# Optimization experiments

Hardware: AMD Instinct MI355X
Metric: run time of the kernel (lower is better)

Reference implementation:

```python
import jax, jax.numpy as jnp
import numpy as np

H = 50  # hidden_layer_size

def _lstm_layer(x, Wih, Whh, bih, bhh):
    # x: [B, T, D_in]; Wih: [4H, D_in]; Whh: [4H, H]; biases: [4H]
    # Precompute input contribution to all gates for every timestep.
    xg = jnp.einsum('btd,gd->btg', x, Wih) + bih + bhh  # [B, T, 4H]
    xg = jnp.transpose(xg, (1, 0, 2))                   # [T, B, 4H] for scan
    B = x.shape[0]
    h0 = jnp.zeros((B, H), x.dtype)
    c0 = jnp.zeros((B, H), x.dtype)

    def step(carry, xt):
        h, c = carry
        g = xt + h @ Whh.T                              # [B, 4H]
        i, f, gg, o = jnp.split(g, 4, axis=-1)          # PyTorch gate order i,f,g,o
        i = jax.nn.sigmoid(i)
        f = jax.nn.sigmoid(f)
        gg = jnp.tanh(gg)
        o = jax.nn.sigmoid(o)
        c = f * c + i * gg
        h = o * jnp.tanh(c)
        return (h, c), h

    (_, _), hs = jax.lax.scan(step, (h0, c0), xg)       # hs: [T, B, H]
    return jnp.transpose(hs, (1, 0, 2))                 # [B, T, H]


def setup_inputs() -> dict:
    key = jax.random.key(0)
    ks = jax.random.split(key, 11)
    B, T, D = 4096, 512, 1
    s = 1.0 / np.sqrt(H)  # PyTorch LSTM init scale
    inp = {
        'x': jax.random.normal(ks[0], (B, T, D), jnp.float32),
        'W_ih0': jax.random.uniform(ks[1], (4 * H, D), jnp.float32, -s, s),
        'W_hh0': jax.random.uniform(ks[2], (4 * H, H), jnp.float32, -s, s),
        'b_ih0': jax.random.uniform(ks[3], (4 * H,), jnp.float32, -s, s),
        'b_hh0': jax.random.uniform(ks[4], (4 * H,), jnp.float32, -s, s),
        'W_ih1': jax.random.uniform(ks[5], (4 * H, H), jnp.float32, -s, s),
        'W_hh1': jax.random.uniform(ks[6], (4 * H, H), jnp.float32, -s, s),
        'b_ih1': jax.random.uniform(ks[7], (4 * H,), jnp.float32, -s, s),
        'b_hh1': jax.random.uniform(ks[8], (4 * H,), jnp.float32, -s, s),
        'fc_W': jax.random.uniform(ks[9], (1, H), jnp.float32, -s, s),
        'fc_b': jax.random.uniform(ks[10], (1,), jnp.float32, -s, s),
    }
    return inp


def reference(x, W_ih0, W_hh0, b_ih0, b_hh0, W_ih1, W_hh1, b_ih1, b_hh1, fc_W, fc_b):
    h1 = _lstm_layer(x, W_ih0, W_hh0, b_ih0, b_hh0)     # [B, T, H]
    h2 = _lstm_layer(h1, W_ih1, W_hh1, b_ih1, b_hh1)    # [B, T, H]
    last = h2[:, -1, :]                                 # [B, H]
    return last @ fc_W.T + fc_b                         # [B, 1]
```

## Files before the change

### kernel.cpp

```cpp
#include <hip/hip_runtime.h>


typedef __attribute__((ext_vector_type(8))) _Float16 half8;
typedef __attribute__((ext_vector_type(4))) float f32x4;

#define LOG2E 1.44269504088896340736f

__device__ __forceinline__ float rcp_(float x) { return __builtin_amdgcn_rcpf(x); }
__device__ __forceinline__ float exp2_(float x) { return __builtin_amdgcn_exp2f(x); }
__device__ __forceinline__ float sigm(float x) {
  return rcp_(1.f + exp2_(-LOG2E * x));
}
__device__ __forceinline__ float tanh_(float x) {
  return 1.f - 2.f * rcp_(1.f + exp2_(2.f * LOG2E * x));
}
__device__ __forceinline__ f32x4 mfma16(half8 a, half8 b, f32x4 c) {
  return __builtin_amdgcn_mfma_f32_16x16x32_f16(a, b, c, 0, 0, 0);
}

union ABu16 { uint4 u; half8 v; };
__device__ __forceinline__ half8 rdfrag(const _Float16* p) {
  ABu16 t;
  t.u = *(const uint4*)p;
  return t.v;
}

__device__ __forceinline__ half8 loadW1(const float* __restrict__ W, int n,
                                        int gate, int kbase, int lg) {
  half8 r;
#pragma unroll
  for (int e = 0; e < 8; ++e) {
    const int k = kbase + 16 * (e >> 2) + 4 * lg + (e & 3);
    const bool v = (n < 50) && (k < 50);
    r[e] = (_Float16)(v ? W[(gate * 50 + n) * 50 + k] : 0.f);
  }
  return r;
}

__global__ __launch_bounds__(768) void lstm2_kernel(
    const float* __restrict__ x,
    const float* __restrict__ Wih0, const float* __restrict__ Whh0,
    const float* __restrict__ bih0, const float* __restrict__ bhh0,
    const float* __restrict__ Wih1, const float* __restrict__ Whh1,
    const float* __restrict__ bih1, const float* __restrict__ bhh1,
    const float* __restrict__ fcW, const float* __restrict__ fcb,
    float* __restrict__ out) {
  const int tid = threadIdx.x;
  const int lane = tid & 63;
  const int wv = tid >> 6;
  const int role = wv >> 2;
  const int wg = wv & 3;
  const int lg = lane >> 4;
  const int l15 = lane & 15;
  const int bbase = blockIdx.x * 16;

  __shared__ __align__(16) _Float16 H0[2][1024], H1[2][1024];
  __shared__ __align__(16) float Pbuf[2][4096];
  __shared__ float xs2[64][16];
  __shared__ float ldspad[10240];

  ((volatile float*)ldspad)[tid] = 0.f;

  for (int i = tid; i < 1024; i += 768) {
    ((unsigned int*)H0)[i] = 0u;
    ((unsigned int*)H1)[i] = 0u;
  }

  const int lane8 = lane * 8;
  const int u = 16 * wg + l15;
  const bool uv = (u < 50);
  const int woff = ((u >> 5) << 9) + (((u >> 2) & 3) << 7) + ((4 * lg) << 3) +
                   (((u >> 4) & 1) << 2) + (u & 3);
  const int pidx = wg * 256 + lane * 4;

#define STAGE(c)                                                        \
  {                                                                     \
    const int b_ = tid >> 4, fg_ = tid & 15;                            \
    const float4 v_ = *(const float4*)&x[(size_t)(bbase + b_) * 512 +   \
                                         (c) * 64 + 4 * fg_];           \
    xs2[4 * fg_ + 0][b_] = v_.x; xs2[4 * fg_ + 1][b_] = v_.y;           \
    xs2[4 * fg_ + 2][b_] = v_.z; xs2[4 * fg_ + 3][b_] = v_.w;           \
  }

  if (role == 0) {
    half8 W0_0, W1_0, W0_1, W1_1, W0_2, W1_2, W0_3, W1_3;
    float bi_0 = 0.f, bi_1 = 0.f, bi_2 = 0.f, bi_3 = 0.f;
    float wx_0 = 0.f, wx_1 = 0.f, wx_2 = 0.f, wx_3 = 0.f;
    W0_0 = loadW1(Whh0, u, 0, 0, lg);  W1_0 = loadW1(Whh0, u, 0, 32, lg);
    W0_1 = loadW1(Whh0, u, 1, 0, lg);  W1_1 = loadW1(Whh0, u, 1, 32, lg);
    W0_2 = loadW1(Whh0, u, 2, 0, lg);  W1_2 = loadW1(Whh0, u, 2, 32, lg);
    W0_3 = loadW1(Whh0, u, 3, 0, lg);  W1_3 = loadW1(Whh0, u, 3, 32, lg);
    if (uv) {
      bi_0 = bih0[0 * 50 + u] + bhh0[0 * 50 + u]; wx_0 = Wih0[0 * 50 + u];
      bi_1 = bih0[1 * 50 + u] + bhh0[1 * 50 + u]; wx_1 = Wih0[1 * 50 + u];
      bi_2 = bih0[2 * 50 + u] + bhh0[2 * 50 + u]; wx_2 = Wih0[2 * 50 + u];
      bi_3 = bih0[3 * 50 + u] + bhh0[3 * 50 + u]; wx_3 = Wih0[3 * 50 + u];
    }
    float cc0 = 0.f, cc1 = 0.f, cc2 = 0.f, cc3 = 0.f;

#define FIN0(r, xr, WPc)                                              \
    { const float i_ = sigm(ai[r] + (xr) * wx_0);                     \
      const float ff = sigm(af[r] + (xr) * wx_1);                     \
      const float g_ = tanh_(ag[r] + (xr) * wx_2);                    \
      const float o_ = sigm(ao[r] + (xr) * wx_3);                     \
      cc##r = ff * cc##r + i_ * g_;                                   \
      H0[WPc][woff + 8 * (r)] = (_Float16)(o_ * tanh_(cc##r)); }

#define L0STEP(RP, WP, tm)                                            \
    { const half8 f0 = rdfrag(&H0[RP][lane8]);                        \
      const half8 f1 = rdfrag(&H0[RP][512 + lane8]);                  \
      f32x4 ai = {bi_0, bi_0, bi_0, bi_0};                            \
      f32x4 af = {bi_1, bi_1, bi_1, bi_1};                            \
      f32x4 ag = {bi_2, bi_2, bi_2, bi_2};                            \
      f32x4 ao = {bi_3, bi_3, bi_3, bi_3};                            \
      ai = mfma16(f0, W0_0, ai); ai = mfma16(f1, W1_0, ai);           \
      af = mfma16(f0, W0_1, af); af = mfma16(f1, W1_1, af);           \
      ag = mfma16(f0, W0_2, ag); ag = mfma16(f1, W1_2, ag);           \
      ao = mfma16(f0, W0_3, ao); ao = mfma16(f1, W1_3, ao);           \
      const float4 xv = *(const float4*)&xs2[tm][4 * lg];             \
      FIN0(0, xv.x, WP) FIN0(1, xv.y, WP)                             \
      FIN0(2, xv.z, WP) FIN0(3, xv.w, WP) }

    for (int it = 0; it <= 256; ++it) {
      if ((it & 31) == 0 && it < 256) { STAGE(it >> 5) __syncthreads(); }
      if (it < 256) L0STEP(1, 0, ((2 * it) & 63))
      __syncthreads();
      if (it < 256) L0STEP(0, 1, ((2 * it + 1) & 63))
      __syncthreads();
    }
  } else if (role == 1) {
    half8 I0_0, I1_0, I0_1, I1_1, I0_2, I1_2, I0_3, I1_3;
    I0_0 = loadW1(Wih1, u, 0, 0, lg);  I1_0 = loadW1(Wih1, u, 0, 32, lg);
    I0_1 = loadW1(Wih1, u, 1, 0, lg);  I1_1 = loadW1(Wih1, u, 1, 32, lg);
    I0_2 = loadW1(Wih1, u, 2, 0, lg);  I1_2 = loadW1(Wih1, u, 2, 32, lg);
    I0_3 = loadW1(Wih1, u, 3, 0, lg);  I1_3 = loadW1(Wih1, u, 3, 32, lg);

#define ISTEP(RP, WPp)                                                \
    { const half8 f0 = rdfrag(&H0[RP][lane8]);                        \
      const half8 f1 = rdfrag(&H0[RP][512 + lane8]);                  \
      f32x4 a0 = {0.f, 0.f, 0.f, 0.f};                                \
      f32x4 a1 = a0, a2 = a0, a3 = a0;                                \
      a0 = mfma16(f0, I0_0, a0); a0 = mfma16(f1, I1_0, a0);           \
      a1 = mfma16(f0, I0_1, a1); a1 = mfma16(f1, I1_1, a1);           \
      a2 = mfma16(f0, I0_2, a2); a2 = mfma16(f1, I1_2, a2);           \
      a3 = mfma16(f0, I0_3, a3); a3 = mfma16(f1, I1_3, a3);           \
      *(f32x4*)&Pbuf[WPp][pidx]        = a0;                          \
      *(f32x4*)&Pbuf[WPp][1024 + pidx] = a1;                          \
      *(f32x4*)&Pbuf[WPp][2048 + pidx] = a2;                          \
      *(f32x4*)&Pbuf[WPp][3072 + pidx] = a3; }

    for (int it = 0; it <= 256; ++it) {
      if ((it & 31) == 0 && it < 256) { __syncthreads(); }
      if (it >= 1) ISTEP(1, 1)
      __syncthreads();
      if (it < 256) ISTEP(0, 0)
      __syncthreads();
    }
  } else {
    half8 R0_0, R1_0, R0_1, R1_1, R0_2, R1_2, R0_3, R1_3;
    float bi_0 = 0.f, bi_1 = 0.f, bi_2 = 0.f, bi_3 = 0.f;
    R0_0 = loadW1(Whh1, u, 0, 0, lg);  R1_0 = loadW1(Whh1, u, 0, 32, lg);
    R0_1 = loadW1(Whh1, u, 1, 0, lg);  R1_1 = loadW1(Whh1, u, 1, 32, lg);
    R0_2 = loadW1(Whh1, u, 2, 0, lg);  R1_2 = loadW1(Whh1, u, 2, 32, lg);
    R0_3 = loadW1(Whh1, u, 3, 0, lg);  R1_3 = loadW1(Whh1, u, 3, 32, lg);
    if (uv) {
      bi_0 = bih1[0 * 50 + u] + bhh1[0 * 50 + u];
      bi_1 = bih1[1 * 50 + u] + bhh1[1 * 50 + u];
      bi_2 = bih1[2 * 50 + u] + bhh1[2 * 50 + u];
      bi_3 = bih1[3 * 50 + u] + bhh1[3 * 50 + u];
    }
    float cc0 = 0.f, cc1 = 0.f, cc2 = 0.f, cc3 = 0.f;

#define FINR2(r, WH)                                                  \
    { const float i_ = sigm(ai[r] + p0[r]);                           \
      const float ff = sigm(af[r] + p1[r]);                           \
      const float g_ = tanh_(ag[r] + p2[r]);                          \
      const float o_ = sigm(ao[r] + p3[r]);                           \
      cc##r = ff * cc##r + i_ * g_;                                   \
      H1[WH][woff + 8 * (r)] = (_Float16)(o_ * tanh_(cc##r)); }

#define RSTEP(PP, RH, WH)                                             \
    { const half8 g0 = rdfrag(&H1[RH][lane8]);                        \
      const half8 g1 = rdfrag(&H1[RH][512 + lane8]);                  \
      const f32x4 p0 = *(const f32x4*)&Pbuf[PP][pidx];                \
      const f32x4 p1 = *(const f32x4*)&Pbuf[PP][1024 + pidx];         \
      const f32x4 p2 = *(const f32x4*)&Pbuf[PP][2048 + pidx];         \
      const f32x4 p3 = *(const f32x4*)&Pbuf[PP][3072 + pidx];         \
      f32x4 ai = {bi_0, bi_0, bi_0, bi_0};                            \
      f32x4 af = {bi_1, bi_1, bi_1, bi_1};                            \
      f32x4 ag = {bi_2, bi_2, bi_2, bi_2};                            \
      f32x4 ao = {bi_3, bi_3, bi_3, bi_3};                            \
      ai = mfma16(g0, R0_0, ai); ai = mfma16(g1, R1_0, ai);           \
      af = mfma16(g0, R0_1, af); af = mfma16(g1, R1_1, af);           \
      ag = mfma16(g0, R0_2, ag); ag = mfma16(g1, R1_2, ag);           \
      ao = mfma16(g0, R0_3, ao); ao = mfma16(g1, R1_3, ao);           \
      FINR2(0, WH) FINR2(1, WH) FINR2(2, WH) FINR2(3, WH) }

    for (int it = 0; it <= 256; ++it) {
      if ((it & 31) == 0 && it < 256) { __syncthreads(); }
      if (it >= 1) RSTEP(0, 1, 0)
      __syncthreads();
      if (it >= 1) RSTEP(1, 0, 1)
      __syncthreads();
    }
  }

  if (tid < 16) {
    float s = fcb[0];
    for (int j = 0; j < 50; ++j) {
      const int idx = ((j >> 5) << 9) + (((j >> 2) & 3) << 7) + (tid << 3) +
                      (((j >> 4) & 1) << 2) + (j & 3);
      s += fcW[j] * (float)H1[1][idx];
    }
    out[bbase + tid] = s;
  }
}

extern "C" void kernel_launch(void* const* d_in, const int* in_sizes, int n_in,
                              void* d_out, int out_size, void* d_ws, size_t ws_size,
                              hipStream_t stream) {
  const float* x    = (const float*)d_in[0];
  const float* Wih0 = (const float*)d_in[1];
  const float* Whh0 = (const float*)d_in[2];
  const float* bih0 = (const float*)d_in[3];
  const float* bhh0 = (const float*)d_in[4];
  const float* Wih1 = (const float*)d_in[5];
  const float* Whh1 = (const float*)d_in[6];
  const float* bih1 = (const float*)d_in[7];
  const float* bhh1 = (const float*)d_in[8];
  const float* fcW  = (const float*)d_in[9];
  const float* fcb  = (const float*)d_in[10];
  float* out = (float*)d_out;

  const int B = out_size;
  const int blocks = B / 16;
  lstm2_kernel<<<dim3(blocks), dim3(768), 0, stream>>>(
      x, Wih0, Whh0, bih0, bhh0, Wih1, Whh1, bih1, bhh1, fcW, fcb, out);
}
```

Baseline: 390.4 us.

## Split layer-1 input projection across two wave groups with separate partial buffers

The block grows from 768 to 1024 threads so that a fourth wave group exists. The layer-1 input projection W_ih1·h0 is split by K-half across two roles, each doing 4 MFMAs into its own LDS buffer (PA/PB). The recurrent role then sums both partials. The goal is to halve the per-step MFMA chain of the projection roles so it is not the critical path between barriers. In exchange, LDS holds an extra partial buffer (offset by shrinking the padding), the recurrent role does more LDS reads, more waves take part in every barrier, and occupancy is pinned via waves_per_eu. Bias vectors are also hoisted and used directly as MFMA accumulators.

```diff
diff --git a/kernel.cpp b/kernel.cpp
--- a/kernel.cpp
+++ b/kernel.cpp
@@ -37,7 +37,9 @@
   return r;
 }
 
-__global__ __launch_bounds__(768) void lstm2_kernel(
+__global__ __launch_bounds__(1024)
+__attribute__((amdgpu_waves_per_eu(4, 4)))
+void lstm2_kernel(
     const float* __restrict__ x,
     const float* __restrict__ Wih0, const float* __restrict__ Whh0,
     const float* __restrict__ bih0, const float* __restrict__ bhh0,
@@ -55,15 +57,15 @@
   const int bbase = blockIdx.x * 16;
 
   __shared__ __align__(16) _Float16 H0[2][1024], H1[2][1024];
-  __shared__ __align__(16) float Pbuf[2][4096];
+  __shared__ __align__(16) float PA[2][4096], PB[2][4096];
   __shared__ float xs2[64][16];
-  __shared__ float ldspad[10240];
-
-  ((volatile float*)ldspad)[tid] = 0.f;
-
-  for (int i = tid; i < 1024; i += 768) {
-    ((unsigned int*)H0)[i] = 0u;
-    ((unsigned int*)H1)[i] = 0u;
+  __shared__ float ldspad[1600];
+
+  ((volatile float*)ldspad)[tid & 1023] = 0.f;
+
+  {
+    ((unsigned int*)H0)[tid] = 0u;
+    ((unsigned int*)H1)[tid] = 0u;
   }
 
   const int lane8 = lane * 8;
@@ -96,6 +98,10 @@
       bi_2 = bih0[2 * 50 + u] + bhh0[2 * 50 + u]; wx_2 = Wih0[2 * 50 + u];
       bi_3 = bih0[3 * 50 + u] + bhh0[3 * 50 + u]; wx_3 = Wih0[3 * 50 + u];
     }
+    const f32x4 b4_0 = {bi_0, bi_0, bi_0, bi_0};
+    const f32x4 b4_1 = {bi_1, bi_1, bi_1, bi_1};
+    const f32x4 b4_2 = {bi_2, bi_2, bi_2, bi_2};
+    const f32x4 b4_3 = {bi_3, bi_3, bi_3, bi_3};
     float cc0 = 0.f, cc1 = 0.f, cc2 = 0.f, cc3 = 0.f;
 
 #define FIN0(r, xr, WPc)                                              \
@@ -109,14 +115,10 @@
 #define L0STEP(RP, WP, tm)                                            \
     { const half8 f0 = rdfrag(&H0[RP][lane8]);                        \
       const half8 f1 = rdfrag(&H0[RP][512 + lane8]);                  \
-      f32x4 ai = {bi_0, bi_0, bi_0, bi_0};                            \
-      f32x4 af = {bi_1, bi_1, bi_1, bi_1};                            \
-      f32x4 ag = {bi_2, bi_2, bi_2, bi_2};                            \
-      f32x4 ao = {bi_3, bi_3, bi_3, bi_3};                            \
-      ai = mfma16(f0, W0_0, ai); ai = mfma16(f1, W1_0, ai);           \
-      af = mfma16(f0, W0_1, af); af = mfma16(f1, W1_1, af);           \
-      ag = mfma16(f0, W0_2, ag); ag = mfma16(f1, W1_2, ag);           \
-      ao = mfma16(f0, W0_3, ao); ao = mfma16(f1, W1_3, ao);           \
+      f32x4 ai = mfma16(f0, W0_0, b4_0); ai = mfma16(f1, W1_0, ai);   \
+      f32x4 af = mfma16(f0, W0_1, b4_1); af = mfma16(f1, W1_1, af);   \
+      f32x4 ag = mfma16(f0, W0_2, b4_2); ag = mfma16(f1, W1_2, ag);   \
+      f32x4 ao = mfma16(f0, W0_3, b4_3); ao = mfma16(f1, W1_3, ao);   \
       const float4 xv = *(const float4*)&xs2[tm][4 * lg];             \
       FIN0(0, xv.x, WP) FIN0(1, xv.y, WP)                             \
       FIN0(2, xv.z, WP) FIN0(3, xv.w, WP) }
@@ -129,31 +131,53 @@
       __syncthreads();
     }
   } else if (role == 1) {
-    half8 I0_0, I1_0, I0_1, I1_1, I0_2, I1_2, I0_3, I1_3;
-    I0_0 = loadW1(Wih1, u, 0, 0, lg);  I1_0 = loadW1(Wih1, u, 0, 32, lg);
-    I0_1 = loadW1(Wih1, u, 1, 0, lg);  I1_1 = loadW1(Wih1, u, 1, 32, lg);
-    I0_2 = loadW1(Wih1, u, 2, 0, lg);  I1_2 = loadW1(Wih1, u, 2, 32, lg);
-    I0_3 = loadW1(Wih1, u, 3, 0, lg);  I1_3 = loadW1(Wih1, u, 3, 32, lg);
-
-#define ISTEP(RP, WPp)                                                \
+    half8 I0_0 = loadW1(Wih1, u, 0, 0, lg);
+    half8 I0_1 = loadW1(Wih1, u, 1, 0, lg);
+    half8 I0_2 = loadW1(Wih1, u, 2, 0, lg);
+    half8 I0_3 = loadW1(Wih1, u, 3, 0, lg);
+
+#define I0STEP(RP, WPp)                                               \
     { const half8 f0 = rdfrag(&H0[RP][lane8]);                        \
-      const half8 f1 = rdfrag(&H0[RP][512 + lane8]);                  \
-      f32x4 a0 = {0.f, 0.f, 0.f, 0.f};                                \
-      f32x4 a1 = a0, a2 = a0, a3 = a0;                                \
-      a0 = mfma16(f0, I0_0, a0); a0 = mfma16(f1, I1_0, a0);           \
-      a1 = mfma16(f0, I0_1, a1); a1 = mfma16(f1, I1_1, a1);           \
-      a2 = mfma16(f0, I0_2, a2); a2 = mfma16(f1, I1_2, a2);           \
-      a3 = mfma16(f0, I0_3, a3); a3 = mfma16(f1, I1_3, a3);           \
-      *(f32x4*)&Pbuf[WPp][pidx]        = a0;                          \
-      *(f32x4*)&Pbuf[WPp][1024 + pidx] = a1;                          \
-      *(f32x4*)&Pbuf[WPp][2048 + pidx] = a2;                          \
-      *(f32x4*)&Pbuf[WPp][3072 + pidx] = a3; }
+      const f32x4 z = {0.f, 0.f, 0.f, 0.f};                           \
+      const f32x4 a0 = mfma16(f0, I0_0, z);                           \
+      const f32x4 a1 = mfma16(f0, I0_1, z);                           \
+      const f32x4 a2 = mfma16(f0, I0_2, z);                           \
+      const f32x4 a3 = mfma16(f0, I0_3, z);                           \
+      *(f32x4*)&PA[WPp][pidx]        = a0;                            \
+      *(f32x4*)&PA[WPp][1024 + pidx] = a1;                            \
+      *(f32x4*)&PA[WPp][2048 + pidx] = a2;                            \
+      *(f32x4*)&PA[WPp][3072 + pidx] = a3; }
 
     for (int it = 0; it <= 256; ++it) {
       if ((it & 31) == 0 && it < 256) { __syncthreads(); }
-      if (it >= 1) ISTEP(1, 1)
-      __syncthreads();
-      if (it < 256) ISTEP(0, 0)
+      if (it >= 1) I0STEP(1, 1)
+      __syncthreads();
+      if (it < 256) I0STEP(0, 0)
+      __syncthreads();
+    }
+  } else if (role == 2) {
+    half8 I1_0 = loadW1(Wih1, u, 0, 32, lg);
+    half8 I1_1 = loadW1(Wih1, u, 1, 32, lg);
+    half8 I1_2 = loadW1(Wih1, u, 2, 32, lg);
+    half8 I1_3 = loadW1(Wih1, u, 3, 32, lg);
+
+#define I1STEP(RP, WPp)                                               \
+    { const half8 f1 = rdfrag(&H0[RP][512 + lane8]);                  \
+      const f32x4 z = {0.f, 0.f, 0.f, 0.f};                           \
+      const f32x4 a0 = mfma16(f1, I1_0, z);                           \
+      const f32x4 a1 = mfma16(f1, I1_1, z);                           \
+      const f32x4 a2 = mfma16(f1, I1_2, z);                           \
+      const f32x4 a3 = mfma16(f1, I1_3, z);                           \
+      *(f32x4*)&PB[WPp][pidx]        = a0;                            \
+      *(f32x4*)&PB[WPp][1024 + pidx] = a1;                            \
+      *(f32x4*)&PB[WPp][2048 + pidx] = a2;                            \
+      *(f32x4*)&PB[WPp][3072 + pidx] = a3; }
+
+    for (int it = 0; it <= 256; ++it) {
+      if ((it & 31) == 0 && it < 256) { __syncthreads(); }
+      if (it >= 1) I1STEP(1, 1)
+      __syncthreads();
+      if (it < 256) I1STEP(0, 0)
       __syncthreads();
     }
   } else {
@@ -169,31 +193,35 @@
       bi_2 = bih1[2 * 50 + u] + bhh1[2 * 50 + u];
       bi_3 = bih1[3 * 50 + u] + bhh1[3 * 50 + u];
     }
+    const f32x4 b4_0 = {bi_0, bi_0, bi_0, bi_0};
+    const f32x4 b4_1 = {bi_1, bi_1, bi_1, bi_1};
+    const f32x4 b4_2 = {bi_2, bi_2, bi_2, bi_2};
+    const f32x4 b4_3 = {bi_3, bi_3, bi_3, bi_3};
     float cc0 = 0.f, cc1 = 0.f, cc2 = 0.f, cc3 = 0.f;
 
 #define FINR2(r, WH)                                                  \
-    { const float i_ = sigm(ai[r] + p0[r]);                           \
-      const float ff = sigm(af[r] + p1[r]);                           \
-      const float g_ = tanh_(ag[r] + p2[r]);                          \
-      const float o_ = sigm(ao[r] + p3[r]);                           \
+    { const float i_ = sigm(ai[r] + pa0[r] + pb0[r]);                 \
+      const float ff = sigm(af[r] + pa1[r] + pb1[r]);                 \
+      const float g_ = tanh_(ag[r] + pa2[r] + pb2[r]);                \
+      const float o_ = sigm(ao[r] + pa3[r] + pb3[r]);                 \
       cc##r = ff * cc##r + i_ * g_;                                   \
       H1[WH][woff + 8 * (r)] = (_Float16)(o_ * tanh_(cc##r)); }
 
 #define RSTEP(PP, RH, WH)                                             \
     { const half8 g0 = rdfrag(&H1[RH][lane8]);                        \
       const half8 g1 = rdfrag(&H1[RH][512 + lane8]);                  \
-      const f32x4 p0 = *(const f32x4*)&Pbuf[PP][pidx];                \
-      const f32x4 p1 = *(const f32x4*)&Pbuf[PP][1024 + pidx];         \
-      const f32x4 p2 = *(const f32x4*)&Pbuf[PP][2048 + pidx];         \
-      const f32x4 p3 = *(const f32x4*)&Pbuf[PP][3072 + pidx];         \
-      f32x4 ai = {bi_0, bi_0, bi_0, bi_0};                            \
-      f32x4 af = {bi_1, bi_1, bi_1, bi_1};                            \
-      f32x4 ag = {bi_2, bi_2, bi_2, bi_2};                            \
-      f32x4 ao = {bi_3, bi_3, bi_3, bi_3};                            \
-      ai = mfma16(g0, R0_0, ai); ai = mfma16(g1, R1_0, ai);           \
-      af = mfma16(g0, R0_1, af); af = mfma16(g1, R1_1, af);           \
-      ag = mfma16(g0, R0_2, ag); ag = mfma16(g1, R1_2, ag);           \
-      ao = mfma16(g0, R0_3, ao); ao = mfma16(g1, R1_3, ao);           \
+      const f32x4 pa0 = *(const f32x4*)&PA[PP][pidx];                 \
+      const f32x4 pa1 = *(const f32x4*)&PA[PP][1024 + pidx];          \
+      const f32x4 pa2 = *(const f32x4*)&PA[PP][2048 + pidx];          \
+      const f32x4 pa3 = *(const f32x4*)&PA[PP][3072 + pidx];          \
+      const f32x4 pb0 = *(const f32x4*)&PB[PP][pidx];                 \
+      const f32x4 pb1 = *(const f32x4*)&PB[PP][1024 + pidx];          \
+      const f32x4 pb2 = *(const f32x4*)&PB[PP][2048 + pidx];          \
+      const f32x4 pb3 = *(const f32x4*)&PB[PP][3072 + pidx];          \
+      f32x4 ai = mfma16(g0, R0_0, b4_0); ai = mfma16(g1, R1_0, ai);   \
+      f32x4 af = mfma16(g0, R0_1, b4_1); af = mfma16(g1, R1_1, af);   \
+      f32x4 ag = mfma16(g0, R0_2, b4_2); ag = mfma16(g1, R1_2, ag);   \
+      f32x4 ao = mfma16(g0, R0_3, b4_3); ao = mfma16(g1, R1_3, ao);   \
       FINR2(0, WH) FINR2(1, WH) FINR2(2, WH) FINR2(3, WH) }
 
     for (int it = 0; it <= 256; ++it) {
@@ -234,6 +262,6 @@
 
   const int B = out_size;
   const int blocks = B / 16;
-  lstm2_kernel<<<dim3(blocks), dim3(768), 0, stream>>>(
+  lstm2_kernel<<<dim3(blocks), dim3(1024), 0, stream>>>(
       x, Wih0, Whh0, bih0, bhh0, Wih1, Whh1, bih1, bhh1, fcW, fcb, out);
 }
```

New measurement: 420.6 us. +7.7%, slower.
